# Kernel optimization log

Measured on AMD Instinct MI355X. Metric: run time of the kernel, lower is better.

## Reference

```python
import jax, jax.numpy as jnp
import numpy as np

# Predictive-coding graph message passing (PCGraphConv core compute).
# Single-graph edge list (edge_src -> edge_dst) with one scalar weight per edge,
# tiled over the batch (weights.repeat(1, batchsize) in the original).
# PredictionMessagePassing: mu_i = sum_{e: dst(e)=i} w_e * f(x_{src(e)})
# ValueMessagePassing:      dx_j = -eps_j + f'(x_j) * sum_{e: src(e)=j} w_e * eps_{dst(e)}
# with eps = x - mu and f = tanh.

N_PER_GRAPH = 4096
E_PER_GRAPH = 524288
BATCH = 32


def setup_inputs() -> dict:
    key = jax.random.key(0)
    k1, k2, k3, k4 = jax.random.split(key, 4)
    x = jax.random.normal(k1, (BATCH * N_PER_GRAPH,), dtype=jnp.float32)
    weights = jax.random.normal(k2, (E_PER_GRAPH,), dtype=jnp.float32) * (1.0 / np.sqrt(N_PER_GRAPH))
    edge_src = jax.random.randint(k3, (E_PER_GRAPH,), 0, N_PER_GRAPH, dtype=jnp.int32)
    edge_dst = jax.random.randint(k4, (E_PER_GRAPH,), 0, N_PER_GRAPH, dtype=jnp.int32)
    return {"x": x, "weights": weights, "edge_src": edge_src, "edge_dst": edge_dst,
            "batch_size": BATCH, "num_vertices": N_PER_GRAPH}


def reference(x, weights, edge_src, edge_dst, batch_size, num_vertices):
    B, N = batch_size, num_vertices
    BN = B * N
    # Tile single-graph edges across the batch with per-graph node offsets.
    offs = (jnp.arange(B, dtype=edge_src.dtype) * N)[:, None]        # [B,1]
    src = (edge_src[None, :] + offs).reshape(-1)                     # [B*E]
    dst = (edge_dst[None, :] + offs).reshape(-1)                     # [B*E]
    w = jnp.tile(weights, B)                                         # [B*E]

    fx = jnp.tanh(x)                                                 # f(x)
    # Predictions: gather f(x) at src, weight per edge, scatter-add at dst.
    mu = jax.ops.segment_sum(w * fx[src], dst, num_segments=BN)      # [B*N]
    eps = x - mu                                                     # errors
    fprime = 1.0 - fx * fx                                           # f'(x)
    # Value update: backward flow of errors along edges.
    dx = -eps + fprime * jax.ops.segment_sum(w * eps[dst], src, num_segments=BN)
    return jnp.stack([mu, dx])                                       # [2, B*N]
```

## Files before the change

kernel.cpp:

```cpp
#include <hip/hip_runtime.h>


static constexpr int kB = 32, kLogB = 5;
static constexpr int kT = 8;
static constexpr int kNumBins = 512;
static constexpr int kChunkE = 2048;
static constexpr int kSlice = 20;
static constexpr int kStageCap = 1280;
static constexpr int kPad = 36;
static constexpr int kMaxRows = 256;

__device__ __forceinline__ unsigned short f2bf(float f) {
  unsigned u = __float_as_uint(f);
  u += 0x7fffu + ((u >> 16) & 1u);
  return (unsigned short)(u >> 16);
}
__device__ __forceinline__ float bf2f(unsigned h) {
  return __uint_as_float(h << 16);
}
__device__ __forceinline__ unsigned pack_rec(int other, int local, unsigned short wb) {
  return ((unsigned)other << 19) | ((unsigned)local << 16) | (unsigned)wb;
}

__global__ void __launch_bounds__(1024) k_binit(
    const float* __restrict__ x, const float* __restrict__ w,
    const int* __restrict__ esrc, const int* __restrict__ edst,
    float* __restrict__ x_t, float* __restrict__ fx_t,
    unsigned* __restrict__ binsA, unsigned* __restrict__ binsB,
    unsigned short* __restrict__ cntA, unsigned short* __restrict__ cntB,
    int N, int E, int nrows) {
  __shared__ int cA[kNumBins], cB[kNumBins];
  __shared__ float tile[32][65];
  int tid = threadIdx.x, blk = blockIdx.x;

  if (blk < nrows) {
    for (int t = tid; t < kNumBins; t += 1024) { cA[t] = 0; cB[t] = 0; }
    __syncthreads();
    int e0 = blk * kChunkE;
#pragma unroll
    for (int k = 0; k < kChunkE / 1024; k++) {
      int e = e0 + k * 1024 + tid;
      if (e < E) {
        int s = esrc[e], d = edst[e];
        unsigned short wb = f2bf(w[e]);
        int slotA = atomicAdd(&cA[d >> 3], 1);
        if (slotA < kSlice)
          binsA[((size_t)blk * kNumBins + (d >> 3)) * kSlice + slotA] =
              pack_rec(s, d & 7, wb);
        int slotB = atomicAdd(&cB[s >> 3], 1);
        if (slotB < kSlice)
          binsB[((size_t)blk * kNumBins + (s >> 3)) * kSlice + slotB] =
              pack_rec(d, s & 7, wb);
      }
    }
    __syncthreads();
    for (int t = tid; t < kNumBins; t += 1024) {
      cntA[(size_t)blk * kNumBins + t] = (unsigned short)min(cA[t], kSlice);
      cntB[(size_t)blk * kNumBins + t] = (unsigned short)min(cB[t], kSlice);
    }
  }

  if (blk < (N >> 6)) {
    int n0 = blk * 64;
    for (int k = tid; k < 32 * 64; k += 1024) {
      int b = k >> 6, n = k & 63;
      tile[b][n] = x[b * N + n0 + n];
    }
    __syncthreads();
    for (int k = tid; k < 64 * 32; k += 1024) {
      int n = k >> 5, b = k & 31;
      float xv = tile[b][n];
      int j = (n0 + n) * kB + b;
      x_t[j] = xv;
      fx_t[j] = tanhf(xv);
    }
  }
}

__global__ void __launch_bounds__(1024) k_accum(
    const unsigned* __restrict__ bins, const unsigned short* __restrict__ cnt,
    const float* __restrict__ vals, const float* __restrict__ x_t,
    const float* __restrict__ fx_t, float* __restrict__ eps_t,
    float* __restrict__ out, int N, int nrows, int mode) {
  __shared__ float rep[32 * kT * kPad];
  __shared__ unsigned stg[kStageCap];
  __shared__ int cntL[kMaxRows];
  __shared__ int scan[kMaxRows];
  int tid = threadIdx.x, t = blockIdx.x;
  int b = tid & 31, slot = tid >> 5;
  float* my = rep + slot * (kT * kPad);
#pragma unroll
  for (int l = 0; l < kT; l++) my[l * kPad + b] = 0.0f;

  if (tid < kMaxRows) {
    int c = (tid < nrows) ? (int)cnt[(size_t)tid * kNumBins + t] : 0;
    cntL[tid] = c;
    scan[tid] = c;
  }
  __syncthreads();
  for (int off = 1; off < kMaxRows; off <<= 1) {
    int v = 0;
    if (tid < kMaxRows && tid >= off) v = scan[tid - off];
    __syncthreads();
    if (tid < kMaxRows && tid >= off) scan[tid] += v;
    __syncthreads();
  }
  int T = min(scan[kMaxRows - 1], kStageCap);

  for (int r = slot; r < nrows; r += 32) {
    int c = cntL[r];
    int base = scan[r] - c;
    if (b < c) {
      int p = base + b;
      if (p < kStageCap)
        stg[p] = bins[((size_t)r * kNumBins + t) * kSlice + b];
    }
  }
  __syncthreads();

  int i = slot;
  unsigned r0 = (i      < T) ? stg[i]      : 0u;
  unsigned r1 = (i + 32 < T) ? stg[i + 32] : 0u;
  unsigned r2 = (i + 64 < T) ? stg[i + 64] : 0u;
  unsigned r3 = (i + 96 < T) ? stg[i + 96] : 0u;
  float v0 = (i      < T) ? vals[((r0 >> 19) << kLogB) + b] : 0.0f;
  float v1 = (i + 32 < T) ? vals[((r1 >> 19) << kLogB) + b] : 0.0f;
  float v2 = (i + 64 < T) ? vals[((r2 >> 19) << kLogB) + b] : 0.0f;
  while (i < T) {
    unsigned r4 = (i + 128 < T) ? stg[i + 128] : 0u;
    float v3 = (i + 96 < T) ? vals[((r3 >> 19) << kLogB) + b] : 0.0f;
    my[((r0 >> 16) & 7) * kPad + b] += bf2f(r0 & 0xffffu) * v0;
    r0 = r1; r1 = r2; r2 = r3; r3 = r4;
    v0 = v1; v1 = v2; v2 = v3;
    i += 32;
  }
  __syncthreads();

  if (tid < kT * kB) {
    int local = tid & 7, bb = tid >> 3;
    float s = 0.0f;
#pragma unroll
    for (int sl = 0; sl < 32; sl++) s += rep[sl * (kT * kPad) + local * kPad + bb];
    int n = t * kT + local;
    int j = n * kB + bb;
    if (mode == 0) {
      out[bb * N + n] = s;
      eps_t[j] = x_t[j] - s;
    } else {
      float fx = fx_t[j];
      out[bb * N + n] = fmaf(1.0f - fx * fx, s, -eps_t[j]);
    }
  }
}

extern "C" void kernel_launch(void* const* d_in, const int* in_sizes, int n_in,
                              void* d_out, int out_size, void* d_ws, size_t ws_size,
                              hipStream_t stream) {
  const float* x    = (const float*)d_in[0];
  const float* w    = (const float*)d_in[1];
  const int*   esrc = (const int*)d_in[2];
  const int*   edst = (const int*)d_in[3];

  int BN = in_sizes[0];
  int E  = in_sizes[1];
  int N  = BN / kB;
  int nrows = (E + kChunkE - 1) / kChunkE;

  float* ws    = (float*)d_ws;
  float* x_t   = ws;
  float* fx_t  = ws + (size_t)BN;
  float* eps_t = ws + 2 * (size_t)BN;
  unsigned short* cntA = (unsigned short*)(ws + 3 * (size_t)BN);
  unsigned short* cntB = cntA + (size_t)kMaxRows * kNumBins;
  unsigned* binsA = (unsigned*)(cntB + (size_t)kMaxRows * kNumBins);
  unsigned* binsB = binsA + (size_t)kMaxRows * kNumBins * kSlice;

  float* out_mu = (float*)d_out;
  float* out_dx = (float*)d_out + BN;

  int nblk1 = max(nrows, N >> 6);

  k_binit<<<nblk1, 1024, 0, stream>>>(x, w, esrc, edst, x_t, fx_t,
                                      binsA, binsB, cntA, cntB, N, E, nrows);
  k_accum<<<kNumBins, 1024, 0, stream>>>(binsA, cntA, fx_t, x_t, fx_t,
                                         eps_t, out_mu, N, nrows, 0);
  k_accum<<<kNumBins, 1024, 0, stream>>>(binsB, cntB, eps_t, x_t, fx_t,
                                         eps_t, out_dx, N, nrows, 1);
}
```

Before: 110.3 us.

## Bin edges into contiguous per-bin buckets via global atomic cursors

Replaces the per-chunk fixed-slot bin layout with one contiguous bucket per destination bin. Each block reserves space with a global atomicAdd on a per-bin cursor after a local shared-memory histogram. The accumulate kernel then reads records straight from global memory, dropping the count load, prefix scan and shared staging. This adds a memset launch and global atomics. The order of records becomes nondeterministic, so float summation order varies between runs.

```diff
diff --git a/kernel.cpp b/kernel.cpp
--- a/kernel.cpp
+++ b/kernel.cpp
@@ -5,10 +5,8 @@
 static constexpr int kT = 8;
 static constexpr int kNumBins = 512;
 static constexpr int kChunkE = 2048;
-static constexpr int kSlice = 20;
-static constexpr int kStageCap = 1280;
+static constexpr int kCap = 1408;
 static constexpr int kPad = 36;
-static constexpr int kMaxRows = 256;
 
 __device__ __forceinline__ unsigned short f2bf(float f) {
   unsigned u = __float_as_uint(f);
@@ -27,37 +25,47 @@
     const int* __restrict__ esrc, const int* __restrict__ edst,
     float* __restrict__ x_t, float* __restrict__ fx_t,
     unsigned* __restrict__ binsA, unsigned* __restrict__ binsB,
-    unsigned short* __restrict__ cntA, unsigned short* __restrict__ cntB,
-    int N, int E, int nrows) {
-  __shared__ int cA[kNumBins], cB[kNumBins];
+    int* __restrict__ cursA, int* __restrict__ cursB, int N, int E) {
+  __shared__ int histA[kNumBins], histB[kNumBins];
+  __shared__ int baseA[kNumBins], baseB[kNumBins];
   __shared__ float tile[32][65];
   int tid = threadIdx.x, blk = blockIdx.x;
 
-  if (blk < nrows) {
-    for (int t = tid; t < kNumBins; t += 1024) { cA[t] = 0; cB[t] = 0; }
-    __syncthreads();
-    int e0 = blk * kChunkE;
-#pragma unroll
-    for (int k = 0; k < kChunkE / 1024; k++) {
-      int e = e0 + k * 1024 + tid;
-      if (e < E) {
-        int s = esrc[e], d = edst[e];
-        unsigned short wb = f2bf(w[e]);
-        int slotA = atomicAdd(&cA[d >> 3], 1);
-        if (slotA < kSlice)
-          binsA[((size_t)blk * kNumBins + (d >> 3)) * kSlice + slotA] =
-              pack_rec(s, d & 7, wb);
-        int slotB = atomicAdd(&cB[s >> 3], 1);
-        if (slotB < kSlice)
-          binsB[((size_t)blk * kNumBins + (s >> 3)) * kSlice + slotB] =
-              pack_rec(d, s & 7, wb);
-      }
-    }
-    __syncthreads();
-    for (int t = tid; t < kNumBins; t += 1024) {
-      cntA[(size_t)blk * kNumBins + t] = (unsigned short)min(cA[t], kSlice);
-      cntB[(size_t)blk * kNumBins + t] = (unsigned short)min(cB[t], kSlice);
-    }
+  if (tid < kNumBins) { histA[tid] = 0; histB[tid] = 0; }
+  __syncthreads();
+  int e0 = blk * kChunkE;
+  int k0 = tid, k1 = tid + 1024;
+  int s0 = 0, d0 = 0, s1 = 0, d1 = 0;
+  unsigned short w0 = 0, w1 = 0;
+  int a0 = 0, b0 = 0, a1 = 0, b1 = 0;
+  bool h0 = e0 + k0 < E, h1 = e0 + k1 < E;
+  if (h0) {
+    s0 = esrc[e0 + k0]; d0 = edst[e0 + k0]; w0 = f2bf(w[e0 + k0]);
+    a0 = atomicAdd(&histA[d0 >> 3], 1);
+    b0 = atomicAdd(&histB[s0 >> 3], 1);
+  }
+  if (h1) {
+    s1 = esrc[e0 + k1]; d1 = edst[e0 + k1]; w1 = f2bf(w[e0 + k1]);
+    a1 = atomicAdd(&histA[d1 >> 3], 1);
+    b1 = atomicAdd(&histB[s1 >> 3], 1);
+  }
+  __syncthreads();
+  if (tid < kNumBins) {
+    baseA[tid] = atomicAdd(&cursA[tid], histA[tid]);
+    baseB[tid] = atomicAdd(&cursB[tid], histB[tid]);
+  }
+  __syncthreads();
+  if (h0) {
+    int bin = d0 >> 3; int p = baseA[bin] + a0;
+    if (p < kCap) binsA[(size_t)bin * kCap + p] = pack_rec(s0, d0 & 7, w0);
+    bin = s0 >> 3; p = baseB[bin] + b0;
+    if (p < kCap) binsB[(size_t)bin * kCap + p] = pack_rec(d0, s0 & 7, w0);
+  }
+  if (h1) {
+    int bin = d1 >> 3; int p = baseA[bin] + a1;
+    if (p < kCap) binsA[(size_t)bin * kCap + p] = pack_rec(s1, d1 & 7, w1);
+    bin = s1 >> 3; p = baseB[bin] + b1;
+    if (p < kCap) binsB[(size_t)bin * kCap + p] = pack_rec(d1, s1 & 7, w1);
   }
 
   if (blk < (N >> 6)) {
@@ -78,56 +86,29 @@
 }
 
 __global__ void __launch_bounds__(1024) k_accum(
-    const unsigned* __restrict__ bins, const unsigned short* __restrict__ cnt,
+    const unsigned* __restrict__ bins, const int* __restrict__ cursors,
     const float* __restrict__ vals, const float* __restrict__ x_t,
     const float* __restrict__ fx_t, float* __restrict__ eps_t,
-    float* __restrict__ out, int N, int nrows, int mode) {
+    float* __restrict__ out, int N, int mode) {
   __shared__ float rep[32 * kT * kPad];
-  __shared__ unsigned stg[kStageCap];
-  __shared__ int cntL[kMaxRows];
-  __shared__ int scan[kMaxRows];
   int tid = threadIdx.x, t = blockIdx.x;
   int b = tid & 31, slot = tid >> 5;
   float* my = rep + slot * (kT * kPad);
 #pragma unroll
   for (int l = 0; l < kT; l++) my[l * kPad + b] = 0.0f;
-
-  if (tid < kMaxRows) {
-    int c = (tid < nrows) ? (int)cnt[(size_t)tid * kNumBins + t] : 0;
-    cntL[tid] = c;
-    scan[tid] = c;
-  }
-  __syncthreads();
-  for (int off = 1; off < kMaxRows; off <<= 1) {
-    int v = 0;
-    if (tid < kMaxRows && tid >= off) v = scan[tid - off];
-    __syncthreads();
-    if (tid < kMaxRows && tid >= off) scan[tid] += v;
-    __syncthreads();
-  }
-  int T = min(scan[kMaxRows - 1], kStageCap);
-
-  for (int r = slot; r < nrows; r += 32) {
-    int c = cntL[r];
-    int base = scan[r] - c;
-    if (b < c) {
-      int p = base + b;
-      if (p < kStageCap)
-        stg[p] = bins[((size_t)r * kNumBins + t) * kSlice + b];
-    }
-  }
-  __syncthreads();
+  int T = min(cursors[t], kCap);
+  const unsigned* bp = bins + (size_t)t * kCap;
 
   int i = slot;
-  unsigned r0 = (i      < T) ? stg[i]      : 0u;
-  unsigned r1 = (i + 32 < T) ? stg[i + 32] : 0u;
-  unsigned r2 = (i + 64 < T) ? stg[i + 64] : 0u;
-  unsigned r3 = (i + 96 < T) ? stg[i + 96] : 0u;
+  unsigned r0 = (i      < T) ? bp[i]      : 0u;
+  unsigned r1 = (i + 32 < T) ? bp[i + 32] : 0u;
+  unsigned r2 = (i + 64 < T) ? bp[i + 64] : 0u;
+  unsigned r3 = (i + 96 < T) ? bp[i + 96] : 0u;
   float v0 = (i      < T) ? vals[((r0 >> 19) << kLogB) + b] : 0.0f;
   float v1 = (i + 32 < T) ? vals[((r1 >> 19) << kLogB) + b] : 0.0f;
   float v2 = (i + 64 < T) ? vals[((r2 >> 19) << kLogB) + b] : 0.0f;
   while (i < T) {
-    unsigned r4 = (i + 128 < T) ? stg[i + 128] : 0u;
+    unsigned r4 = (i + 128 < T) ? bp[i + 128] : 0u;
     float v3 = (i + 96 < T) ? vals[((r3 >> 19) << kLogB) + b] : 0.0f;
     my[((r0 >> 16) & 7) * kPad + b] += bf2f(r0 & 0xffffu) * v0;
     r0 = r1; r1 = r2; r2 = r3; r3 = r4;
@@ -164,26 +145,26 @@
   int BN = in_sizes[0];
   int E  = in_sizes[1];
   int N  = BN / kB;
-  int nrows = (E + kChunkE - 1) / kChunkE;
 
   float* ws    = (float*)d_ws;
   float* x_t   = ws;
   float* fx_t  = ws + (size_t)BN;
   float* eps_t = ws + 2 * (size_t)BN;
-  unsigned short* cntA = (unsigned short*)(ws + 3 * (size_t)BN);
-  unsigned short* cntB = cntA + (size_t)kMaxRows * kNumBins;
-  unsigned* binsA = (unsigned*)(cntB + (size_t)kMaxRows * kNumBins);
-  unsigned* binsB = binsA + (size_t)kMaxRows * kNumBins * kSlice;
+  int*   cursA = (int*)(ws + 3 * (size_t)BN);
+  int*   cursB = cursA + kNumBins;
+  unsigned* binsA = (unsigned*)(cursB + kNumBins);
+  unsigned* binsB = binsA + (size_t)kNumBins * kCap;
 
   float* out_mu = (float*)d_out;
   float* out_dx = (float*)d_out + BN;
 
-  int nblk1 = max(nrows, N >> 6);
+  int nblk_bin = (E + kChunkE - 1) / kChunkE;
 
-  k_binit<<<nblk1, 1024, 0, stream>>>(x, w, esrc, edst, x_t, fx_t,
-                                      binsA, binsB, cntA, cntB, N, E, nrows);
-  k_accum<<<kNumBins, 1024, 0, stream>>>(binsA, cntA, fx_t, x_t, fx_t,
-                                         eps_t, out_mu, N, nrows, 0);
-  k_accum<<<kNumBins, 1024, 0, stream>>>(binsB, cntB, eps_t, x_t, fx_t,
-                                         eps_t, out_dx, N, nrows, 1);
+  hipMemsetAsync(cursA, 0, 2 * kNumBins * sizeof(int), stream);
+  k_binit<<<nblk_bin, 1024, 0, stream>>>(x, w, esrc, edst, x_t, fx_t,
+                                         binsA, binsB, cursA, cursB, N, E);
+  k_accum<<<kNumBins, 1024, 0, stream>>>(binsA, cursA, fx_t, x_t, fx_t,
+                                         eps_t, out_mu, N, 0);
+  k_accum<<<kNumBins, 1024, 0, stream>>>(binsB, cursB, eps_t, x_t, fx_t,
+                                         eps_t, out_dx, N, 1);
 }
```

After: 110.6 us. No clear change (+0.3%).
